# Kernel optimization log

Measured on AMD Instinct MI355X. Metric: run time of the kernel, lower is better.

Reference implementation:

```python
import jax, jax.numpy as jnp
import numpy as np

BETA = 0.5
LAMBDA = 0.5
EPS = 1e-24


def setup_inputs() -> dict:
    key = jax.random.key(0)
    k1, k2 = jax.random.split(key)
    seq = jax.random.normal(k1, (32, 512, 128), dtype=jnp.float32)
    fism_items = jax.random.normal(k2, (32, 2048, 128), dtype=jnp.float32)
    return {"seq": seq, "fism_items": fism_items}


def reference(seq, fism_items):
    # scores: [B, L, N]
    w = jnp.einsum('bld,bnd->bln', seq, fism_items)
    w_shift = w - jnp.max(w, axis=-1, keepdims=True)
    exp_w = jnp.exp(w_shift)
    exp_sum = jnp.sum(exp_w, axis=-1, keepdims=True)
    if BETA != 1.0:
        exp_sum = jnp.power(exp_sum, jnp.float32(BETA))
    att = exp_w / (exp_sum + EPS)  # power-normalized softmax
    att_vecs = jnp.einsum('bln,bnd->bld', att, fism_items)
    if LAMBDA < 1:
        return seq * (1.0 - LAMBDA) + seq * att_vecs * LAMBDA
    return seq * att_vecs
```

## Files before the change

kernel.cpp:

```cpp
#include <hip/hip_runtime.h>
#include <hip/hip_bf16.h>
#include <math.h>

typedef _Float16 half8  __attribute__((ext_vector_type(8)));
typedef _Float16 half4v __attribute__((ext_vector_type(4)));
typedef __fp16   fp16x2 __attribute__((ext_vector_type(2)));
typedef float    f32x4  __attribute__((ext_vector_type(4)));

#define DDIM 128
#define LQ   512
#define NKV  2048
#define KVB  64
#define NIT  8

union U32H2 { unsigned u; fp16x2 h; };
union H8W   { unsigned u[4]; half8 h; };

__device__ __forceinline__ int swzk(int row) { return (row & 7) << 3; }
__device__ __forceinline__ int swzv(int d)   { return ((d ^ (d >> 4)) & 7) << 3; }

__global__ __launch_bounds__(512, 2)
void gattn(const float* __restrict__ seq, const float* __restrict__ fism,
           float* __restrict__ out)
{
  const int tid  = threadIdx.x;
  const int lane = tid & 63;
  const int wv   = tid >> 6;
  const int wq   = wv & 1;
  const int kvq  = wv >> 1;
  const int q16  = lane & 15;
  const int g    = lane >> 4;

  const int swz = (blockIdx.x & 7) * 32 + (blockIdx.x >> 3);
  const int b   = swz >> 3;
  const int qb  = (swz & 7) * 64;

  const float* seqB = seq  + (size_t)b * LQ * DDIM;
  const float* fisB = fism + (size_t)b * NKV * DDIM;
  float*       outB = out  + (size_t)b * LQ * DDIM;

  __shared__ _Float16 Ksh[4][KVB * DDIM];
  __shared__ _Float16 VTsh[4][DDIM * KVB];
  __shared__ float    stats[4][2][2][16][3];

  half8 qf[2][4];
  #pragma unroll
  for (int qs = 0; qs < 2; ++qs) {
    const int qrow = qb + wq * 32 + qs * 16 + q16;
    #pragma unroll
    for (int c = 0; c < 4; ++c) {
      const float* p = seqB + (size_t)qrow * DDIM + c * 32 + g * 8;
      float4 a  = *(const float4*)p;
      float4 b2 = *(const float4*)(p + 4);
      half8 h;
      h[0]=(_Float16)a.x;  h[1]=(_Float16)a.y;  h[2]=(_Float16)a.z;  h[3]=(_Float16)a.w;
      h[4]=(_Float16)b2.x; h[5]=(_Float16)b2.y; h[6]=(_Float16)b2.z; h[7]=(_Float16)b2.w;
      qf[qs][c] = h;
    }
  }

  const int sp   = tid >> 3;
  const int dgrp = tid & 7;
  const int qstg = sp >> 4;
  const int spc  = sp & 15;

  f32x4 acc[2][8];
  #pragma unroll
  for (int qs = 0; qs < 2; ++qs)
    #pragma unroll
    for (int i = 0; i < 8; ++i) { f32x4 z = {0.f,0.f,0.f,0.f}; acc[qs][i] = z; }

  float m_run[2] = {-INFINITY, -INFINITY};
  float tmax[2]  = {-INFINITY, -INFINITY};
  float S_run[2] = {0.f, 0.f};

  auto write_stage = [&](const float4* v) {
    #pragma unroll
    for (int r = 0; r < 4; ++r) {
      const int row = 4*spc + r;
      #pragma unroll
      for (int hh = 0; hh < 2; ++hh) {
        const float4 x = v[r*4 + hh*2];
        const float4 y = v[r*4 + hh*2 + 1];
        half8 h;
        h[0]=(_Float16)x.x; h[1]=(_Float16)x.y; h[2]=(_Float16)x.z; h[3]=(_Float16)x.w;
        h[4]=(_Float16)y.x; h[5]=(_Float16)y.y; h[6]=(_Float16)y.z; h[7]=(_Float16)y.w;
        const int idx = row*DDIM + ((dgrp*16 + hh*8) ^ swzk(row));
        *(half8*)&Ksh[qstg][idx] = h;
      }
    }
    #pragma unroll
    for (int k = 0; k < 16; ++k) {
      const int d = dgrp*16 + k;
      half4v pk;
      #pragma unroll
      for (int r = 0; r < 4; ++r)
        pk[r] = (_Float16)(((const float*)&v[r*4 + (k>>2)])[k&3]);
      const int idx = d*KVB + ((4*spc) ^ swzv(d));
      *(half4v*)&VTsh[qstg][idx] = pk;
    }
  };

  auto load_glb = [&](float4* v, int t) {
    const float* src = fisB + (size_t)(qstg*(NKV/4) + t*KVB) * DDIM;
    #pragma unroll
    for (int r = 0; r < 4; ++r)
      #pragma unroll
      for (int k = 0; k < 4; ++k)
        v[r*4+k] = *(const float4*)(src + (size_t)(4*spc + r)*DDIM + dgrp*16 + k*4);
  };

  {
    float4 stg[16];
    load_glb(stg, 0);
    write_stage(stg);
  }

  for (int t = 0; t < NIT; ++t) {
    __syncthreads();
    float4 nxt[16];
    const bool have = (t + 1 < NIT);
    if (have) load_glb(nxt, t + 1);

    f32x4 sv[2][4];
    #pragma unroll
    for (int ns = 0; ns < 4; ++ns) {
      f32x4 x0 = {0.f,0.f,0.f,0.f}, x1 = {0.f,0.f,0.f,0.f};
      const int row = ns*16 + q16;
      #pragma unroll
      for (int c = 0; c < 4; ++c) {
        const int idx = row*DDIM + ((c*32 + g*8) ^ swzk(row));
        half8 kf = *(const half8*)&Ksh[kvq][idx];
        x0 = __builtin_amdgcn_mfma_f32_16x16x32_f16(kf, qf[0][c], x0, 0, 0, 0);
        x1 = __builtin_amdgcn_mfma_f32_16x16x32_f16(kf, qf[1][c], x1, 0, 0, 0);
      }
      sv[0][ns] = x0; sv[1][ns] = x1;
    }

    unsigned upk[2][4][2];
    #pragma unroll
    for (int qs = 0; qs < 2; ++qs) {
      float cmax = sv[qs][0][0];
      #pragma unroll
      for (int ns = 0; ns < 4; ++ns)
        #pragma unroll
        for (int i = 0; i < 4; ++i)
          cmax = fmaxf(cmax, sv[qs][ns][i]);
      cmax = fmaxf(cmax, __shfl_xor(cmax, 16));
      cmax = fmaxf(cmax, __shfl_xor(cmax, 32));
      tmax[qs] = fmaxf(tmax[qs], cmax);
      if (__any(cmax > m_run[qs] + 8.f)) {
        const float mn = fmaxf(m_run[qs], cmax);
        const float sc = __expf(m_run[qs] - mn);
        S_run[qs] *= sc;
        m_run[qs] = mn;
        const float s0 = __shfl(sc, (g<<4) | (4*g + 0));
        const float s1 = __shfl(sc, (g<<4) | (4*g + 1));
        const float s2 = __shfl(sc, (g<<4) | (4*g + 2));
        const float s3 = __shfl(sc, (g<<4) | (4*g + 3));
        const f32x4 scv = {s0, s1, s2, s3};
        #pragma unroll
        for (int dsu = 0; dsu < 8; ++dsu) acc[qs][dsu] *= scv;
      }
      float lsum = 0.f;
      #pragma unroll
      for (int ns = 0; ns < 4; ++ns)
        #pragma unroll
        for (int i = 0; i < 4; ++i) {
          const float p = __expf(sv[qs][ns][i] - m_run[qs]);
          sv[qs][ns][i] = p;
          lsum += p;
        }
      lsum += __shfl_xor(lsum, 16);
      lsum += __shfl_xor(lsum, 32);
      S_run[qs] += lsum;

      #pragma unroll
      for (int ns = 0; ns < 4; ++ns) {
        U32H2 u0, u1;
        u0.h = __builtin_amdgcn_cvt_pkrtz(sv[qs][ns][0], sv[qs][ns][1]);
        u1.h = __builtin_amdgcn_cvt_pkrtz(sv[qs][ns][2], sv[qs][ns][3]);
        upk[qs][ns][0] = u0.u; upk[qs][ns][1] = u1.u;
      }
    }

    #pragma unroll
    for (int c = 0; c < 2; ++c) {
      H8W aw0, aw1;
      #pragma unroll
      for (int tt = 0; tt < 4; ++tt) {
        const int src = q16 + 16 * ((g & 1) * 2 + (tt >> 1));
        const unsigned lo0 = (unsigned)__shfl((int)upk[0][2*c  ][tt & 1], src);
        const unsigned hi0 = (unsigned)__shfl((int)upk[0][2*c+1][tt & 1], src);
        const unsigned lo1 = (unsigned)__shfl((int)upk[1][2*c  ][tt & 1], src);
        const unsigned hi1 = (unsigned)__shfl((int)upk[1][2*c+1][tt & 1], src);
        aw0.u[tt] = (g < 2) ? lo0 : hi0;
        aw1.u[tt] = (g < 2) ? lo1 : hi1;
      }
      const half8 pa0 = aw0.h, pa1 = aw1.h;
      #pragma unroll
      for (int dsu = 0; dsu < 8; ++dsu) {
        const int d = dsu*16 + q16;
        const int idx = d*KVB + ((c*32 + g*8) ^ swzv(d));
        half8 vf = *(const half8*)&VTsh[kvq][idx];
        acc[0][dsu] = __builtin_amdgcn_mfma_f32_16x16x32_f16(pa0, vf, acc[0][dsu], 0, 0, 0);
        acc[1][dsu] = __builtin_amdgcn_mfma_f32_16x16x32_f16(pa1, vf, acc[1][dsu], 0, 0, 0);
      }
    }

    __syncthreads();
    if (have) write_stage(nxt);
  }

  __syncthreads();

  float* Kf  = (float*)&Ksh[0][0];
  float* VTf = (float*)&VTsh[0][0];
  if (kvq != 0) {
    #pragma unroll
    for (int qs = 0; qs < 2; ++qs) {
      const int rgn = (((kvq - 1) * 2 + wq) << 1) | qs;
      float* base = (rgn < 8) ? (Kf + rgn * 2048) : (VTf + (rgn - 8) * 2048);
      float* p = base + lane * 32;
      #pragma unroll
      for (int dsu = 0; dsu < 8; ++dsu)
        *(f32x4*)&p[(dsu * 4) ^ ((lane & 7) << 2)] = acc[qs][dsu];
      if (g == 0) {
        stats[kvq][wq][qs][q16][0] = m_run[qs];
        stats[kvq][wq][qs][q16][1] = S_run[qs];
        stats[kvq][wq][qs][q16][2] = tmax[qs];
      }
    }
  }
  __syncthreads();

  if (kvq == 0) {
    #pragma unroll
    for (int qs = 0; qs < 2; ++qs) {
      float mj[4], Sj[4], tj[4];
      mj[0] = m_run[qs]; Sj[0] = S_run[qs]; tj[0] = tmax[qs];
      #pragma unroll
      for (int j = 1; j < 4; ++j) {
        mj[j] = stats[j][wq][qs][q16][0];
        Sj[j] = stats[j][wq][qs][q16][1];
        tj[j] = stats[j][wq][qs][q16][2];
      }
      const float M = fmaxf(fmaxf(tj[0], tj[1]), fmaxf(tj[2], tj[3]));
      float aj[4], den = 0.f;
      #pragma unroll
      for (int j = 0; j < 4; ++j) { aj[j] = __expf(mj[j] - M); den += aj[j] * Sj[j]; }
      const float rs = rsqrtf(den);
      float fr[4][4];
      #pragma unroll
      for (int j = 0; j < 4; ++j) {
        const float fj = aj[j] * rs;
        #pragma unroll
        for (int i = 0; i < 4; ++i)
          fr[j][i] = __shfl(fj, (g<<4) | (4*g + i));
      }
      #pragma unroll
      for (int dsu = 0; dsu < 8; ++dsu) {
        f32x4 av = acc[qs][dsu];
        av *= (f32x4){fr[0][0], fr[0][1], fr[0][2], fr[0][3]};
        #pragma unroll
        for (int j = 1; j < 4; ++j) {
          const int rgn = (((j - 1) * 2 + wq) << 1) | qs;
          const float* base = (rgn < 8) ? (Kf + rgn * 2048) : (VTf + (rgn - 8) * 2048);
          const f32x4 pj = *(const f32x4*)&base[lane*32 + ((dsu * 4) ^ ((lane & 7) << 2))];
          av += pj * (f32x4){fr[j][0], fr[j][1], fr[j][2], fr[j][3]};
        }
        #pragma unroll
        for (int i = 0; i < 4; ++i) {
          const int qrow = qb + wq*32 + qs*16 + 4*g + i;
          const int d = dsu*16 + q16;
          const float s = seqB[(size_t)qrow * DDIM + d];
          outB[(size_t)qrow * DDIM + d] = 0.5f * s * (1.f + av[i]);
        }
      }
    }
  }
}

extern "C" void kernel_launch(void* const* d_in, const int* in_sizes, int n_in,
                              void* d_out, int out_size, void* d_ws, size_t ws_size,
                              hipStream_t stream) {
  const float* seq  = (const float*)d_in[0];
  const float* fism = (const float*)d_in[1];
  float* out = (float*)d_out;
  gattn<<<dim3(256), dim3(512), 0, stream>>>(seq, fism, out);
}
```

Measured before the change: 52.41 us.

## Switch attention MFMAs to 32x32x16 tiles with permlane32 reductions

Replaces the 16x16x32 MFMA tiling with 32x32x16 MFMAs so each wave handles 32 query rows in a single tile, with the score matrix transposed so each lane owns one query row. Row max and sum reductions become mostly in-register followed by a permlane32 swap, replacing shuffles, and the P operand is rebuilt with permlane32_swap instead of many ds_bpermute shuffles. The shared-memory layouts and swizzles for K and V^T change to match, and the epilogue writes float4 vectors. The goal is fewer cross-lane ops and more work per MFMA, at the cost of new layout logic that must be exactly correct.

```diff
diff --git a/kernel.cpp b/kernel.cpp
--- a/kernel.cpp
+++ b/kernel.cpp
@@ -6,6 +6,8 @@
 typedef _Float16 half4v __attribute__((ext_vector_type(4)));
 typedef __fp16   fp16x2 __attribute__((ext_vector_type(2)));
 typedef float    f32x4  __attribute__((ext_vector_type(4)));
+typedef float    f32x16 __attribute__((ext_vector_type(16)));
+typedef int      i32x2v __attribute__((ext_vector_type(2)));
 
 #define DDIM 128
 #define LQ   512
@@ -14,10 +16,16 @@
 #define NIT  8
 
 union U32H2 { unsigned u; fp16x2 h; };
-union H8W   { unsigned u[4]; half8 h; };
-
-__device__ __forceinline__ int swzk(int row) { return (row & 7) << 3; }
-__device__ __forceinline__ int swzv(int d)   { return ((d ^ (d >> 4)) & 7) << 3; }
+union PW    { unsigned u[4]; half8 h; };
+
+__device__ __forceinline__ float xmax64(float v) {
+  i32x2v r = __builtin_amdgcn_permlane32_swap(__float_as_int(v), __float_as_int(v), false, false);
+  return fmaxf(__int_as_float(r[0]), __int_as_float(r[1]));
+}
+__device__ __forceinline__ float xsum64(float v) {
+  i32x2v r = __builtin_amdgcn_permlane32_swap(__float_as_int(v), __float_as_int(v), false, false);
+  return __int_as_float(r[0]) + __int_as_float(r[1]);
+}
 
 __global__ __launch_bounds__(512, 2)
 void gattn(const float* __restrict__ seq, const float* __restrict__ fism,
@@ -28,8 +36,8 @@
   const int wv   = tid >> 6;
   const int wq   = wv & 1;
   const int kvq  = wv >> 1;
-  const int q16  = lane & 15;
-  const int g    = lane >> 4;
+  const int l31  = lane & 31;
+  const int hi   = lane >> 5;
 
   const int swz = (blockIdx.x & 7) * 32 + (blockIdx.x >> 3);
   const int b   = swz >> 3;
@@ -40,22 +48,21 @@
   float*       outB = out  + (size_t)b * LQ * DDIM;
 
   __shared__ _Float16 Ksh[4][KVB * DDIM];
-  __shared__ _Float16 VTsh[4][DDIM * KVB];
-  __shared__ float    stats[4][2][2][16][3];
-
-  half8 qf[2][4];
-  #pragma unroll
-  for (int qs = 0; qs < 2; ++qs) {
-    const int qrow = qb + wq * 32 + qs * 16 + q16;
-    #pragma unroll
-    for (int c = 0; c < 4; ++c) {
-      const float* p = seqB + (size_t)qrow * DDIM + c * 32 + g * 8;
+  __shared__ _Float16 VTsh[4][(DDIM/2) * 128];
+  __shared__ float    stats[4][2][32][3];
+
+  half8 qf[8];
+  {
+    const int qrow = qb + wq * 32 + l31;
+    #pragma unroll
+    for (int c = 0; c < 8; ++c) {
+      const float* p = seqB + (size_t)qrow * DDIM + c * 16 + hi * 8;
       float4 a  = *(const float4*)p;
       float4 b2 = *(const float4*)(p + 4);
       half8 h;
       h[0]=(_Float16)a.x;  h[1]=(_Float16)a.y;  h[2]=(_Float16)a.z;  h[3]=(_Float16)a.w;
       h[4]=(_Float16)b2.x; h[5]=(_Float16)b2.y; h[6]=(_Float16)b2.z; h[7]=(_Float16)b2.w;
-      qf[qs][c] = h;
+      qf[c] = h;
     }
   }
 
@@ -64,15 +71,13 @@
   const int qstg = sp >> 4;
   const int spc  = sp & 15;
 
-  f32x4 acc[2][8];
+  f32x16 acc[4];
   #pragma unroll
-  for (int qs = 0; qs < 2; ++qs)
-    #pragma unroll
-    for (int i = 0; i < 8; ++i) { f32x4 z = {0.f,0.f,0.f,0.f}; acc[qs][i] = z; }
-
-  float m_run[2] = {-INFINITY, -INFINITY};
-  float tmax[2]  = {-INFINITY, -INFINITY};
-  float S_run[2] = {0.f, 0.f};
+  for (int dt = 0; dt < 4; ++dt)
+    #pragma unroll
+    for (int i = 0; i < 16; ++i) acc[dt][i] = 0.f;
+
+  float m_run = -INFINITY, tmax = -INFINITY, S_run = 0.f;
 
   auto write_stage = [&](const float4* v) {
     #pragma unroll
@@ -85,18 +90,19 @@
         half8 h;
         h[0]=(_Float16)x.x; h[1]=(_Float16)x.y; h[2]=(_Float16)x.z; h[3]=(_Float16)x.w;
         h[4]=(_Float16)y.x; h[5]=(_Float16)y.y; h[6]=(_Float16)y.z; h[7]=(_Float16)y.w;
-        const int idx = row*DDIM + ((dgrp*16 + hh*8) ^ swzk(row));
+        const int idx = row*DDIM + ((dgrp*16 + hh*8) ^ (8*(row & 15)));
         *(half8*)&Ksh[qstg][idx] = h;
       }
     }
     #pragma unroll
     for (int k = 0; k < 16; ++k) {
       const int d = dgrp*16 + k;
+      const int dRow = d >> 1, dSub = d & 1;
       half4v pk;
       #pragma unroll
       for (int r = 0; r < 4; ++r)
         pk[r] = (_Float16)(((const float*)&v[r*4 + (k>>2)])[k&3]);
-      const int idx = d*KVB + ((4*spc) ^ swzv(d));
+      const int idx = dRow*128 + ((dSub*64 + 4*spc) ^ (8*(dRow & 15)));
       *(half4v*)&VTsh[qstg][idx] = pk;
     }
   };
@@ -122,89 +128,83 @@
     const bool have = (t + 1 < NIT);
     if (have) load_glb(nxt, t + 1);
 
-    f32x4 sv[2][4];
-    #pragma unroll
-    for (int ns = 0; ns < 4; ++ns) {
-      f32x4 x0 = {0.f,0.f,0.f,0.f}, x1 = {0.f,0.f,0.f,0.f};
-      const int row = ns*16 + q16;
-      #pragma unroll
-      for (int c = 0; c < 4; ++c) {
-        const int idx = row*DDIM + ((c*32 + g*8) ^ swzk(row));
+    f32x16 sv[2];
+    #pragma unroll
+    for (int ns = 0; ns < 2; ++ns) {
+      f32x16 x;
+      #pragma unroll
+      for (int i = 0; i < 16; ++i) x[i] = 0.f;
+      const int row = ns*32 + l31;
+      const int sw  = 8*(row & 15);
+      #pragma unroll
+      for (int c = 0; c < 8; ++c) {
+        const int idx = row*DDIM + ((c*16 + hi*8) ^ sw);
         half8 kf = *(const half8*)&Ksh[kvq][idx];
-        x0 = __builtin_amdgcn_mfma_f32_16x16x32_f16(kf, qf[0][c], x0, 0, 0, 0);
-        x1 = __builtin_amdgcn_mfma_f32_16x16x32_f16(kf, qf[1][c], x1, 0, 0, 0);
-      }
-      sv[0][ns] = x0; sv[1][ns] = x1;
-    }
-
-    unsigned upk[2][4][2];
-    #pragma unroll
-    for (int qs = 0; qs < 2; ++qs) {
-      float cmax = sv[qs][0][0];
-      #pragma unroll
-      for (int ns = 0; ns < 4; ++ns)
-        #pragma unroll
-        for (int i = 0; i < 4; ++i)
-          cmax = fmaxf(cmax, sv[qs][ns][i]);
-      cmax = fmaxf(cmax, __shfl_xor(cmax, 16));
-      cmax = fmaxf(cmax, __shfl_xor(cmax, 32));
-      tmax[qs] = fmaxf(tmax[qs], cmax);
-      if (__any(cmax > m_run[qs] + 8.f)) {
-        const float mn = fmaxf(m_run[qs], cmax);
-        const float sc = __expf(m_run[qs] - mn);
-        S_run[qs] *= sc;
-        m_run[qs] = mn;
-        const float s0 = __shfl(sc, (g<<4) | (4*g + 0));
-        const float s1 = __shfl(sc, (g<<4) | (4*g + 1));
-        const float s2 = __shfl(sc, (g<<4) | (4*g + 2));
-        const float s3 = __shfl(sc, (g<<4) | (4*g + 3));
-        const f32x4 scv = {s0, s1, s2, s3};
-        #pragma unroll
-        for (int dsu = 0; dsu < 8; ++dsu) acc[qs][dsu] *= scv;
-      }
-      float lsum = 0.f;
-      #pragma unroll
-      for (int ns = 0; ns < 4; ++ns)
-        #pragma unroll
-        for (int i = 0; i < 4; ++i) {
-          const float p = __expf(sv[qs][ns][i] - m_run[qs]);
-          sv[qs][ns][i] = p;
-          lsum += p;
-        }
-      lsum += __shfl_xor(lsum, 16);
-      lsum += __shfl_xor(lsum, 32);
-      S_run[qs] += lsum;
-
-      #pragma unroll
-      for (int ns = 0; ns < 4; ++ns) {
-        U32H2 u0, u1;
-        u0.h = __builtin_amdgcn_cvt_pkrtz(sv[qs][ns][0], sv[qs][ns][1]);
-        u1.h = __builtin_amdgcn_cvt_pkrtz(sv[qs][ns][2], sv[qs][ns][3]);
-        upk[qs][ns][0] = u0.u; upk[qs][ns][1] = u1.u;
-      }
-    }
-
-    #pragma unroll
-    for (int c = 0; c < 2; ++c) {
-      H8W aw0, aw1;
-      #pragma unroll
-      for (int tt = 0; tt < 4; ++tt) {
-        const int src = q16 + 16 * ((g & 1) * 2 + (tt >> 1));
-        const unsigned lo0 = (unsigned)__shfl((int)upk[0][2*c  ][tt & 1], src);
-        const unsigned hi0 = (unsigned)__shfl((int)upk[0][2*c+1][tt & 1], src);
-        const unsigned lo1 = (unsigned)__shfl((int)upk[1][2*c  ][tt & 1], src);
-        const unsigned hi1 = (unsigned)__shfl((int)upk[1][2*c+1][tt & 1], src);
-        aw0.u[tt] = (g < 2) ? lo0 : hi0;
-        aw1.u[tt] = (g < 2) ? lo1 : hi1;
-      }
-      const half8 pa0 = aw0.h, pa1 = aw1.h;
-      #pragma unroll
-      for (int dsu = 0; dsu < 8; ++dsu) {
-        const int d = dsu*16 + q16;
-        const int idx = d*KVB + ((c*32 + g*8) ^ swzv(d));
-        half8 vf = *(const half8*)&VTsh[kvq][idx];
-        acc[0][dsu] = __builtin_amdgcn_mfma_f32_16x16x32_f16(pa0, vf, acc[0][dsu], 0, 0, 0);
-        acc[1][dsu] = __builtin_amdgcn_mfma_f32_16x16x32_f16(pa1, vf, acc[1][dsu], 0, 0, 0);
+        x = __builtin_amdgcn_mfma_f32_32x32x16_f16(kf, qf[c], x, 0, 0, 0);
+      }
+      sv[ns] = x;
+    }
+
+    float mx[16];
+    #pragma unroll
+    for (int i = 0; i < 16; ++i) mx[i] = fmaxf(sv[0][i], sv[1][i]);
+    #pragma unroll
+    for (int st = 8; st > 0; st >>= 1)
+      #pragma unroll
+      for (int i = 0; i < st; ++i) mx[i] = fmaxf(mx[i], mx[i+st]);
+    const float cmax = xmax64(mx[0]);
+    tmax = fmaxf(tmax, cmax);
+    if (__any(cmax > m_run + 8.f)) {
+      const float mn = fmaxf(m_run, cmax);
+      const float sc = __expf(m_run - mn);
+      S_run *= sc;
+      m_run = mn;
+      #pragma unroll
+      for (int dt = 0; dt < 4; ++dt) acc[dt] *= sc;
+    }
+    float ts[16];
+    #pragma unroll
+    for (int i = 0; i < 16; ++i) {
+      const float p0 = __expf(sv[0][i] - m_run);
+      const float p1 = __expf(sv[1][i] - m_run);
+      sv[0][i] = p0; sv[1][i] = p1;
+      ts[i] = p0 + p1;
+    }
+    #pragma unroll
+    for (int st = 8; st > 0; st >>= 1)
+      #pragma unroll
+      for (int i = 0; i < st; ++i) ts[i] += ts[i+st];
+    S_run += xsum64(ts[0]);
+
+    PW pw[4];
+    #pragma unroll
+    for (int ns = 0; ns < 2; ++ns)
+      #pragma unroll
+      for (int b0 = 0; b0 < 2; ++b0) {
+        U32H2 t0, t1, t2, t3;
+        t0.h = __builtin_amdgcn_cvt_pkrtz(sv[ns][8*b0+0], sv[ns][8*b0+1]);
+        t1.h = __builtin_amdgcn_cvt_pkrtz(sv[ns][8*b0+2], sv[ns][8*b0+3]);
+        t2.h = __builtin_amdgcn_cvt_pkrtz(sv[ns][8*b0+4], sv[ns][8*b0+5]);
+        t3.h = __builtin_amdgcn_cvt_pkrtz(sv[ns][8*b0+6], sv[ns][8*b0+7]);
+        i32x2v r0 = __builtin_amdgcn_permlane32_swap((int)t0.u, (int)t2.u, false, false);
+        i32x2v r1 = __builtin_amdgcn_permlane32_swap((int)t1.u, (int)t3.u, false, false);
+        const int kb = 2*ns + b0;
+        pw[kb].u[0] = (unsigned)r0[0];
+        pw[kb].u[1] = (unsigned)r1[0];
+        pw[kb].u[2] = (unsigned)r0[1];
+        pw[kb].u[3] = (unsigned)r1[1];
+      }
+
+    #pragma unroll
+    for (int dt = 0; dt < 4; ++dt) {
+      const int d    = dt*32 + l31;
+      const int dRow = d >> 1, dSub = d & 1;
+      const int sw   = 8*(dRow & 15);
+      #pragma unroll
+      for (int kb = 0; kb < 4; ++kb) {
+        const int idx = dRow*128 + ((dSub*64 + kb*16 + hi*8) ^ sw);
+        half8 vtf = *(const half8*)&VTsh[kvq][idx];
+        acc[dt] = __builtin_amdgcn_mfma_f32_32x32x16_f16(vtf, pw[kb].h, acc[dt], 0, 0, 0);
       }
     }
 
@@ -217,65 +217,62 @@
   float* Kf  = (float*)&Ksh[0][0];
   float* VTf = (float*)&VTsh[0][0];
   if (kvq != 0) {
-    #pragma unroll
-    for (int qs = 0; qs < 2; ++qs) {
-      const int rgn = (((kvq - 1) * 2 + wq) << 1) | qs;
-      float* base = (rgn < 8) ? (Kf + rgn * 2048) : (VTf + (rgn - 8) * 2048);
-      float* p = base + lane * 32;
-      #pragma unroll
-      for (int dsu = 0; dsu < 8; ++dsu)
-        *(f32x4*)&p[(dsu * 4) ^ ((lane & 7) << 2)] = acc[qs][dsu];
-      if (g == 0) {
-        stats[kvq][wq][qs][q16][0] = m_run[qs];
-        stats[kvq][wq][qs][q16][1] = S_run[qs];
-        stats[kvq][wq][qs][q16][2] = tmax[qs];
-      }
+    const int rgn = (kvq - 1) * 2 + wq;
+    float* base = (rgn < 4) ? (Kf + rgn * 4096) : (VTf + (rgn - 4) * 4096);
+    #pragma unroll
+    for (int dt = 0; dt < 4; ++dt)
+      #pragma unroll
+      for (int rg = 0; rg < 4; ++rg) {
+        f32x4 v = {acc[dt][4*rg+0], acc[dt][4*rg+1], acc[dt][4*rg+2], acc[dt][4*rg+3]};
+        *(f32x4*)&base[lane*64 + (((dt*4+rg) ^ (lane & 15)) * 4)] = v;
+      }
+    if (lane < 32) {
+      stats[kvq][wq][lane][0] = m_run;
+      stats[kvq][wq][lane][1] = S_run;
+      stats[kvq][wq][lane][2] = tmax;
     }
   }
   __syncthreads();
 
   if (kvq == 0) {
-    #pragma unroll
-    for (int qs = 0; qs < 2; ++qs) {
-      float mj[4], Sj[4], tj[4];
-      mj[0] = m_run[qs]; Sj[0] = S_run[qs]; tj[0] = tmax[qs];
-      #pragma unroll
-      for (int j = 1; j < 4; ++j) {
-        mj[j] = stats[j][wq][qs][q16][0];
-        Sj[j] = stats[j][wq][qs][q16][1];
-        tj[j] = stats[j][wq][qs][q16][2];
-      }
-      const float M = fmaxf(fmaxf(tj[0], tj[1]), fmaxf(tj[2], tj[3]));
-      float aj[4], den = 0.f;
-      #pragma unroll
-      for (int j = 0; j < 4; ++j) { aj[j] = __expf(mj[j] - M); den += aj[j] * Sj[j]; }
-      const float rs = rsqrtf(den);
-      float fr[4][4];
-      #pragma unroll
-      for (int j = 0; j < 4; ++j) {
-        const float fj = aj[j] * rs;
-        #pragma unroll
-        for (int i = 0; i < 4; ++i)
-          fr[j][i] = __shfl(fj, (g<<4) | (4*g + i));
-      }
-      #pragma unroll
-      for (int dsu = 0; dsu < 8; ++dsu) {
-        f32x4 av = acc[qs][dsu];
-        av *= (f32x4){fr[0][0], fr[0][1], fr[0][2], fr[0][3]};
+    float mj[4], Sj[4], tj[4];
+    mj[0] = m_run; Sj[0] = S_run; tj[0] = tmax;
+    #pragma unroll
+    for (int j = 1; j < 4; ++j) {
+      mj[j] = stats[j][wq][l31][0];
+      Sj[j] = stats[j][wq][l31][1];
+      tj[j] = stats[j][wq][l31][2];
+    }
+    const float M = fmaxf(fmaxf(tj[0], tj[1]), fmaxf(tj[2], tj[3]));
+    float fj[4], den = 0.f;
+    #pragma unroll
+    for (int j = 0; j < 4; ++j) { fj[j] = __expf(mj[j] - M); den += fj[j] * Sj[j]; }
+    const float rs = rsqrtf(den);
+    #pragma unroll
+    for (int j = 0; j < 4; ++j) fj[j] *= rs;
+
+    const int qrow = qb + wq*32 + l31;
+    #pragma unroll
+    for (int dt = 0; dt < 4; ++dt) {
+      #pragma unroll
+      for (int rg = 0; rg < 4; ++rg) {
+        f32x4 av = {acc[dt][4*rg+0], acc[dt][4*rg+1], acc[dt][4*rg+2], acc[dt][4*rg+3]};
+        av *= fj[0];
         #pragma unroll
         for (int j = 1; j < 4; ++j) {
-          const int rgn = (((j - 1) * 2 + wq) << 1) | qs;
-          const float* base = (rgn < 8) ? (Kf + rgn * 2048) : (VTf + (rgn - 8) * 2048);
-          const f32x4 pj = *(const f32x4*)&base[lane*32 + ((dsu * 4) ^ ((lane & 7) << 2))];
-          av += pj * (f32x4){fr[j][0], fr[j][1], fr[j][2], fr[j][3]};
+          const int rgn = (j - 1) * 2 + wq;
+          const float* base = (rgn < 4) ? (Kf + rgn * 4096) : (VTf + (rgn - 4) * 4096);
+          const f32x4 pj = *(const f32x4*)&base[lane*64 + (((dt*4+rg) ^ (lane & 15)) * 4)];
+          av += pj * fj[j];
         }
-        #pragma unroll
-        for (int i = 0; i < 4; ++i) {
-          const int qrow = qb + wq*32 + qs*16 + 4*g + i;
-          const int d = dsu*16 + q16;
-          const float s = seqB[(size_t)qrow * DDIM + d];
-          outB[(size_t)qrow * DDIM + d] = 0.5f * s * (1.f + av[i]);
-        }
+        const int d0 = dt*32 + rg*8 + hi*4;
+        const float4 s = *(const float4*)&seqB[(size_t)qrow * DDIM + d0];
+        float4 o;
+        o.x = 0.5f * s.x * (1.f + av[0]);
+        o.y = 0.5f * s.y * (1.f + av[1]);
+        o.z = 0.5f * s.z * (1.f + av[2]);
+        o.w = 0.5f * s.w * (1.f + av[3]);
+        *(float4*)&outB[(size_t)qrow * DDIM + d0] = o;
       }
     }
   }
```

New measurement: 61.54 us. +17.4%, slower.
